# Kernel optimization log

Measured on AMD Instinct MI355X. Metric: run time of the kernel, lower is better.

## Reference

```python
import jax, jax.numpy as jnp
import numpy as np

B, N, E = 2, 30000, 120000
IN_F, OUT_F, H = 512, 512, 4
D = OUT_F // H  # head_dim = 128
LN_EPS = 1e-5


def setup_inputs() -> dict:
    key = jax.random.key(0)
    k1, k2, k3, k4 = jax.random.split(key, 4)
    node_features = jax.random.normal(k1, (B, N, IN_F), dtype=jnp.float32)
    edge_index = jax.random.randint(k2, (2, E), 0, N, dtype=jnp.int64)
    # per-head linear transforms (bias=False): W[h] is [in_features, head_dim]
    W = jax.random.normal(k3, (H, IN_F, D), dtype=jnp.float32) / np.sqrt(IN_F)
    # per-head attention vectors a[h] is [2*head_dim] (Linear(2*head_dim,1,bias=False))
    a = jax.random.normal(k4, (H, 2 * D), dtype=jnp.float32) / np.sqrt(2 * D)
    ln_gamma = jnp.ones((OUT_F,), dtype=jnp.float32)
    ln_beta = jnp.zeros((OUT_F,), dtype=jnp.float32)
    return {"node_features": node_features, "edge_index": edge_index,
            "W": W, "a": a, "ln_gamma": ln_gamma, "ln_beta": ln_beta}


def reference(node_features, edge_index, W, a, ln_gamma, ln_beta):
    src, dst = edge_index[0], edge_index[1]
    # all-heads linear transform: [B, H, N, D]
    t = jnp.einsum('bni,hid->bhnd', node_features, W)
    # per-edge gathered features: [B, H, E, D]
    sf = t[:, :, src, :]
    df = t[:, :, dst, :]
    # attention score = [sf ; df] . a  == sf.a_src + df.a_dst  -> [B, H, E]
    scores = (jnp.einsum('bhed,hd->bhe', sf, a[:, :D])
              + jnp.einsum('bhed,hd->bhe', df, a[:, D:]))
    scores = jax.nn.leaky_relu(scores, negative_slope=0.2)
    # NOTE: faithful to source — softmax over ALL edges (dim=-1), not per-dst
    w = jax.nn.softmax(scores, axis=-1)
    # scatter-add aggregation into destination nodes (the Python-loop in torch)
    agg = jnp.zeros_like(t).at[:, :, dst, :].add(w[..., None] * sf)  # [B,H,N,D]
    # concat heads along feature dim (head order preserved)
    out = jnp.transpose(agg, (0, 2, 1, 3)).reshape(node_features.shape[0], N, H * D)
    # LayerNorm over last dim
    mu = jnp.mean(out, axis=-1, keepdims=True)
    var = jnp.mean(jnp.square(out - mu), axis=-1, keepdims=True)
    out = (out - mu) * jax.lax.rsqrt(var + LN_EPS) * ln_gamma + ln_beta
    return out
```

## Files before the change

kernel.cpp:

```cpp
#include <hip/hip_runtime.h>
#include <stdint.h>

#define Bn 2
#define Nn 30000
#define En 120000
#define KIN 512
#define Hh 4
#define Dd 128
#define MROWS 60000
#define MPAD  60032
#define LNEPS 1e-5f
#define EBLK 469

typedef unsigned short u16;
typedef unsigned int   u32;
typedef __attribute__((ext_vector_type(8))) short short8;
typedef __attribute__((ext_vector_type(4))) float f32x4;

__device__ __forceinline__ u16 f2bf(float f) {
    u32 u = __builtin_bit_cast(u32, f);
    u32 r = u + 0x7FFFu + ((u >> 16) & 1u);
    return (u16)(r >> 16);
}
__device__ __forceinline__ float bflo(u32 u) {
    return __builtin_bit_cast(float, u << 16);
}
__device__ __forceinline__ float bfhi(u32 u) {
    return __builtin_bit_cast(float, u & 0xFFFF0000u);
}
__device__ __forceinline__ void ld16(void* lds, const void* g) {
    __builtin_amdgcn_global_load_lds((const __attribute__((address_space(1))) void*)g,
                                     (__attribute__((address_space(3))) void*)lds, 16, 0, 0);
}

#define CVTW_BLKS 1024
__global__ void prep_kernel(const float* __restrict__ W, u16* __restrict__ wbt,
                            const int* __restrict__ ei, int* __restrict__ deg) {
    int blk = blockIdx.x;
    if (blk < CVTW_BLKS) {
        int idx = blk * 256 + threadIdx.x;
        int c = idx >> 9, i = idx & 511;
        int h = c >> 7, d = c & 127;
        wbt[idx] = f2bf(W[h * (KIN * Dd) + i * Dd + d]);
    } else {
        int e = (blk - CVTW_BLKS) * 256 + threadIdx.x;
        if (e < En) atomicAdd(&deg[ei[En + e]], 1);
    }
}

__device__ void scan512(const int* __restrict__ deg, int* __restrict__ offs,
                        int* __restrict__ cursor, int* __restrict__ part) {
    int tid = threadIdx.x;
    const int CH = 59;
    int start = tid * CH;
    int s = 0;
    for (int i = 0; i < CH; i++) {
        int n = start + i;
        if (n < Nn) s += deg[n];
    }
    part[tid] = s;
    __syncthreads();
    for (int off = 1; off < 512; off <<= 1) {
        int xv = (tid >= off) ? part[tid - off] : 0;
        __syncthreads();
        part[tid] += xv;
        __syncthreads();
    }
    int run = part[tid] - s;
    for (int i = 0; i < CH; i++) {
        int n = start + i;
        if (n < Nn) {
            offs[n] = run;
            cursor[n] = run;
            run += deg[n];
        }
    }
    if (tid == 511) offs[Nn] = part[511];
}

#define A_LDS (2 * 128 * 32)
#define B_LDS (2 * 512 * 32)
__launch_bounds__(512)
__global__ void gemm(const float* __restrict__ x, const u16* __restrict__ wbt,
                     const float* __restrict__ ag, u16* __restrict__ t,
                     float* __restrict__ s1g, float* __restrict__ s2g,
                     const int* __restrict__ deg, int* __restrict__ offs,
                     int* __restrict__ cursor) {
    __shared__ __align__(16) u16 smem[A_LDS + B_LDS];
    if (blockIdx.x == 0) { scan512(deg, offs, cursor, (int*)smem); return; }
    u16* As0 = smem;
    u16* As1 = smem + 128 * 32;
    u16* Bs0 = smem + A_LDS;
    u16* Bs1 = smem + A_LDS + 512 * 32;
    const int tid = threadIdx.x;
    const int m0 = (blockIdx.x - 1) * 128;
    const int w = tid >> 6, l = tid & 63;
    const int lr = l & 15, lk = l >> 4;
    const int wrM = (w >> 2) * 64;
    const int h = w & 3;
    const int wc = h * 128;
    const int swz = (lk * 8) ^ ((lr & 6) << 2);
    int aoff[4], boff[8];
    #pragma unroll
    for (int mi = 0; mi < 4; mi++) aoff[mi] = (wrM + mi * 16 + lr) * 32 + swz;
    #pragma unroll
    for (int nj = 0; nj < 8; nj++) boff[nj] = (wc + nj * 16 + lr) * 32 + swz;

    const int arow_u = m0 + (tid >> 2);
    const int arow = arow_u < MROWS ? arow_u : (MROWS - 1);
    const float* xsrc = x + (long)arow * KIN + (tid & 3) * 8;
    const int awr = (tid >> 2) * 32 + (((tid & 3) * 8) ^ (((tid >> 2) & 6) << 2));

    const int grow = tid >> 2, gslot = tid & 3;
    const int gsw = (gslot * 8) ^ ((grow & 6) << 2);
    const u16* bgsrc = wbt + (long)grow * KIN + gsw;
    f32x4 acc[4][8] = {};
    float4 a0A, a1A, a0B, a1B;

#define LOADX(R0, R1, KS)                                           \
    {                                                               \
        R0 = *(const float4*)(xsrc + (KS) * 32);                    \
        R1 = *(const float4*)(xsrc + (KS) * 32 + 4);                \
    }
#define CVTW(BUF, R0, R1)                                           \
    {                                                               \
        short8 o;                                                   \
        o[0] = (short)f2bf(R0.x); o[1] = (short)f2bf(R0.y);         \
        o[2] = (short)f2bf(R0.z); o[3] = (short)f2bf(R0.w);         \
        o[4] = (short)f2bf(R1.x); o[5] = (short)f2bf(R1.y);         \
        o[6] = (short)f2bf(R1.z); o[7] = (short)f2bf(R1.w);         \
        *(short8*)&(BUF)[awr] = o;                                  \
    }

    auto STAGEB = [&](u16* Bb, int k0) {
        #pragma unroll
        for (int i = 0; i < 4; i++)
            ld16(Bb + ((long)(i * 512 + tid)) * 8, bgsrc + (long)i * 128 * KIN + k0);
    };

    LOADX(a0A, a1A, 0);
    LOADX(a0B, a1B, 1);
    STAGEB(Bs0, 0);
    CVTW(As0, a0A, a1A);
    __syncthreads();

    #pragma unroll
    for (int t16 = 0; t16 < 16; t16++) {
        u16* Acur = (t16 & 1) ? As1 : As0;
        u16* Bcur = (t16 & 1) ? Bs1 : Bs0;
        u16* Anext = (t16 & 1) ? As0 : As1;
        u16* Bnext = (t16 & 1) ? Bs0 : Bs1;
        if (t16 < 14) {
            if (t16 & 1) { LOADX(a0B, a1B, t16 + 2); }
            else         { LOADX(a0A, a1A, t16 + 2); }
        }
        if (t16 < 15) STAGEB(Bnext, (t16 + 1) * 32);
        short8 af[4];
        #pragma unroll
        for (int mi = 0; mi < 4; mi++) af[mi] = *(const short8*)&Acur[aoff[mi]];
        #pragma unroll
        for (int nj = 0; nj < 8; nj++) {
            short8 bv = *(const short8*)&Bcur[boff[nj]];
            #pragma unroll
            for (int mi = 0; mi < 4; mi++)
                acc[mi][nj] = __builtin_amdgcn_mfma_f32_16x16x32_bf16(
                    af[mi], bv, acc[mi][nj], 0, 0, 0);
        }
        if (t16 < 15) {
            if (t16 & 1) { CVTW(Anext, a0A, a1A); }
            else         { CVTW(Anext, a0B, a1B); }
        }
        __syncthreads();
    }
#undef LOADX
#undef CVTW

    #pragma unroll
    for (int mi = 0; mi < 4; mi++)
        #pragma unroll
        for (int r = 0; r < 4; r++) {
            int row = m0 + wrM + mi * 16 + lk * 4 + r;
            u16* tp = t + (long)row * 512 + wc + lr;
            #pragma unroll
            for (int nj = 0; nj < 8; nj++)
                tp[nj * 16] = f2bf(acc[mi][nj][r]);
        }
    float a1c[8], a2c[8];
    #pragma unroll
    for (int nj = 0; nj < 8; nj++) {
        int col = nj * 16 + lr;
        a1c[nj] = ag[h * 256 + col];
        a2c[nj] = ag[h * 256 + 128 + col];
    }
    float p1[16], p2[16];
    #pragma unroll
    for (int mi = 0; mi < 4; mi++)
        #pragma unroll
        for (int r = 0; r < 4; r++) {
            float v1 = 0.f, v2 = 0.f;
            #pragma unroll
            for (int nj = 0; nj < 8; nj++) {
                float tv = acc[mi][nj][r];
                v1 += tv * a1c[nj];
                v2 += tv * a2c[nj];
            }
            p1[mi * 4 + r] = v1;
            p2[mi * 4 + r] = v2;
        }
    #pragma unroll
    for (int off = 1; off < 16; off <<= 1)
        #pragma unroll
        for (int i = 0; i < 16; i++) {
            p1[i] += __shfl_xor(p1[i], off, 64);
            p2[i] += __shfl_xor(p2[i], off, 64);
        }
    if (lr == 0) {
        #pragma unroll
        for (int mi = 0; mi < 4; mi++)
            #pragma unroll
            for (int r = 0; r < 4; r++) {
                int row = m0 + wrM + mi * 16 + lk * 4 + r;
                if (row < MROWS) {
                    s1g[(long)row * 4 + h] = p1[mi * 4 + r];
                    s2g[(long)row * 4 + h] = p2[mi * 4 + r];
                }
            }
    }
}

__global__ void edgescatter_kernel(const int* __restrict__ ei, const float* __restrict__ s1,
                                   const float* __restrict__ s2, int* __restrict__ cursor,
                                   int* __restrict__ srcs, float* __restrict__ pw,
                                   float* __restrict__ Zpart) {
    int e = blockIdx.x * 256 + threadIdx.x;
    int tid = threadIdx.x;
    float v[8] = {0.f, 0.f, 0.f, 0.f, 0.f, 0.f, 0.f, 0.f};
    if (e < En) {
        int src = ei[e], dst = ei[En + e];
        #pragma unroll
        for (int b = 0; b < Bn; b++) {
            float4 v1 = *(const float4*)(s1 + ((long)b * Nn + src) * 4);
            float4 v2 = *(const float4*)(s2 + ((long)b * Nn + dst) * 4);
            float s;
            s = v1.x + v2.x; s = s > 0.f ? s : 0.2f * s; v[b * 4 + 0] = __expf(s);
            s = v1.y + v2.y; s = s > 0.f ? s : 0.2f * s; v[b * 4 + 1] = __expf(s);
            s = v1.z + v2.z; s = s > 0.f ? s : 0.2f * s; v[b * 4 + 2] = __expf(s);
            s = v1.w + v2.w; s = s > 0.f ? s : 0.2f * s; v[b * 4 + 3] = __expf(s);
        }
        int pos = atomicAdd(&cursor[dst], 1);
        srcs[pos] = src;
        *(float4*)(pw + (long)pos * 4)        = make_float4(v[0], v[1], v[2], v[3]);
        *(float4*)(pw + ((long)En + pos) * 4) = make_float4(v[4], v[5], v[6], v[7]);
    }
    #pragma unroll
    for (int off = 1; off < 64; off <<= 1)
        #pragma unroll
        for (int i = 0; i < 8; i++)
            v[i] += __shfl_xor(v[i], off, 64);
    __shared__ float red[4][8];
    if ((tid & 63) == 0)
        #pragma unroll
        for (int i = 0; i < 8; i++)
            red[tid >> 6][i] = v[i];
    __syncthreads();
    if (tid < 8)
        Zpart[(long)blockIdx.x * 8 + tid] =
            red[0][tid] + red[1][tid] + red[2][tid] + red[3][tid];
}

__global__ void zreduce_kernel(const float* __restrict__ Zpart, float* __restrict__ invZ) {
    int tid = threadIdx.x;
    int g = tid >> 5, l = tid & 31;
    float s = 0.f;
    for (int i = l; i < EBLK; i += 32)
        s += Zpart[(long)i * 8 + g];
    #pragma unroll
    for (int off = 1; off < 32; off <<= 1)
        s += __shfl_xor(s, off, 64);
    if (l == 0) invZ[g] = 1.0f / s;
}

__launch_bounds__(128)
__global__ void agg_kernel(const u16* __restrict__ t, const int* __restrict__ srcs,
                           const float* __restrict__ pw, const float* __restrict__ invZ,
                           const int* __restrict__ offs,
                           const float* __restrict__ gamma, const float* __restrict__ beta,
                           float* __restrict__ out) {
    int tid = threadIdx.x;
    int b = tid >> 6;
    int l = tid & 63;
    int n = blockIdx.x;
    int h = l >> 4;
    int j0 = offs[n], j1 = offs[n + 1];
    const float* pwb = pw + (long)b * En * 4;
    const u16* tb = t + (long)b * Nn * 512;
    float a0 = 0.f, a1 = 0.f, a2 = 0.f, a3 = 0.f;
    float a4 = 0.f, a5 = 0.f, a6 = 0.f, a7 = 0.f;
    for (int j = j0; j < j1; j += 4) {
        int  jj0 = j,     jj1 = j + 1,  jj2 = j + 2,  jj3 = j + 3;
        bool k1 = jj1 < j1, k2 = jj2 < j1, k3 = jj3 < j1;
        int  i1 = k1 ? jj1 : j0, i2 = k2 ? jj2 : j0, i3 = k3 ? jj3 : j0;
        int s0 = srcs[jj0], s1i = srcs[i1], s2i = srcs[i2], s3i = srcs[i3];
        float w0 = pwb[(long)jj0 * 4 + h];
        float w1 = k1 ? pwb[(long)i1 * 4 + h] : 0.f;
        float w2 = k2 ? pwb[(long)i2 * 4 + h] : 0.f;
        float w3 = k3 ? pwb[(long)i3 * 4 + h] : 0.f;
        uint4 r0 = *(const uint4*)(tb + (long)s0 * 512 + l * 8);
        uint4 r1 = *(const uint4*)(tb + (long)s1i * 512 + l * 8);
        uint4 r2 = *(const uint4*)(tb + (long)s2i * 512 + l * 8);
        uint4 r3 = *(const uint4*)(tb + (long)s3i * 512 + l * 8);
        a0 += w0 * bflo(r0.x) + w1 * bflo(r1.x) + w2 * bflo(r2.x) + w3 * bflo(r3.x);
        a1 += w0 * bfhi(r0.x) + w1 * bfhi(r1.x) + w2 * bfhi(r2.x) + w3 * bfhi(r3.x);
        a2 += w0 * bflo(r0.y) + w1 * bflo(r1.y) + w2 * bflo(r2.y) + w3 * bflo(r3.y);
        a3 += w0 * bfhi(r0.y) + w1 * bfhi(r1.y) + w2 * bfhi(r2.y) + w3 * bfhi(r3.y);
        a4 += w0 * bflo(r0.z) + w1 * bflo(r1.z) + w2 * bflo(r2.z) + w3 * bflo(r3.z);
        a5 += w0 * bfhi(r0.z) + w1 * bfhi(r1.z) + w2 * bfhi(r2.z) + w3 * bfhi(r3.z);
        a6 += w0 * bflo(r0.w) + w1 * bflo(r1.w) + w2 * bflo(r2.w) + w3 * bflo(r3.w);
        a7 += w0 * bfhi(r0.w) + w1 * bfhi(r1.w) + w2 * bfhi(r2.w) + w3 * bfhi(r3.w);
    }
    float invz = invZ[b * 4 + h];
    a0 *= invz; a1 *= invz; a2 *= invz; a3 *= invz;
    a4 *= invz; a5 *= invz; a6 *= invz; a7 *= invz;
    float s  = a0 + a1 + a2 + a3 + a4 + a5 + a6 + a7;
    float ss = a0 * a0 + a1 * a1 + a2 * a2 + a3 * a3
             + a4 * a4 + a5 * a5 + a6 * a6 + a7 * a7;
    #pragma unroll
    for (int off = 1; off < 64; off <<= 1) {
        s  += __shfl_xor(s, off, 64);
        ss += __shfl_xor(ss, off, 64);
    }
    float mean = s * (1.0f / 512.0f);
    float var = ss * (1.0f / 512.0f) - mean * mean;
    var = var < 0.f ? 0.f : var;
    float scale = rsqrtf(var + LNEPS);
    int c = l * 8;
    float4 g0 = *(const float4*)(gamma + c);
    float4 g1 = *(const float4*)(gamma + c + 4);
    float4 b0 = *(const float4*)(beta + c);
    float4 b1 = *(const float4*)(beta + c + 4);
    float4 o0, o1;
    o0.x = (a0 - mean) * scale * g0.x + b0.x;
    o0.y = (a1 - mean) * scale * g0.y + b0.y;
    o0.z = (a2 - mean) * scale * g0.z + b0.z;
    o0.w = (a3 - mean) * scale * g0.w + b0.w;
    o1.x = (a4 - mean) * scale * g1.x + b1.x;
    o1.y = (a5 - mean) * scale * g1.y + b1.y;
    o1.z = (a6 - mean) * scale * g1.z + b1.z;
    o1.w = (a7 - mean) * scale * g1.w + b1.w;
    float* op = out + ((long)b * Nn + n) * 512 + c;
    *(float4*)(op)     = o0;
    *(float4*)(op + 4) = o1;
}

extern "C" void kernel_launch(void* const* d_in, const int* in_sizes, int n_in,
                              void* d_out, int out_size, void* d_ws, size_t ws_size,
                              hipStream_t stream) {
    const float* x     = (const float*)d_in[0];
    const int*   ei    = (const int*)d_in[1];
    const float* W     = (const float*)d_in[2];
    const float* a     = (const float*)d_in[3];
    const float* gamma = (const float*)d_in[4];
    const float* beta  = (const float*)d_in[5];
    float* out = (float*)d_out;

    char* ws = (char*)d_ws;
    size_t off = 0;
    auto alloc = [&](size_t bytes) -> void* {
        void* ptr = ws + off;
        off = (off + bytes + 255) & ~(size_t)255;
        return ptr;
    };
    u16*   wbt    = (u16*)alloc((size_t)512 * 512 * 2);
    u16*   t      = (u16*)alloc((size_t)MPAD * 512 * 2);
    float* s1     = (float*)alloc((size_t)MROWS * 4 * 4);
    float* s2     = (float*)alloc((size_t)MROWS * 4 * 4);
    float* pw     = (float*)alloc((size_t)Bn * En * 4 * 4);
    float* Zpart  = (float*)alloc((size_t)EBLK * 8 * 4);
    float* invZ   = (float*)alloc(8 * 4);
    int*   deg    = (int*)alloc((size_t)Nn * 4);
    int*   offs   = (int*)alloc((size_t)(Nn + 1) * 4);
    int*   cursor = (int*)alloc((size_t)Nn * 4);
    int*   srcs   = (int*)alloc((size_t)En * 4);

    hipMemsetAsync(deg, 0, (size_t)Nn * 4, stream);

    prep_kernel<<<CVTW_BLKS + EBLK, 256, 0, stream>>>(W, wbt, ei, deg);
    gemm<<<470, 512, 0, stream>>>(x, wbt, a, t, s1, s2, deg, offs, cursor);
    edgescatter_kernel<<<EBLK, 256, 0, stream>>>(ei, s1, s2, cursor, srcs, pw, Zpart);
    zreduce_kernel<<<1, 256, 0, stream>>>(Zpart, invZ);
    agg_kernel<<<Nn, 128, 0, stream>>>(t, srcs, pw, invZ, offs, gamma, beta, out);
}
```

Baseline: 361.7 us.

## Fuse all stages into one cooperative persistent kernel with grid syncs

Replaces the memset and five kernel launches with a single cooperative kernel of 256 blocks that runs weight conversion, degree counting, the GEMM, the CSR scan, edge scatter, the Z reduction and aggregation/LayerNorm, separated by grid.sync. This removes launch gaps and the separate Z reduction kernel; the softmax denominator is now accumulated with global atomics. In exchange the GEMM runs on only 256 blocks for 469 tiles, which is about two uneven waves. The scan still sits on a single block, and each grid barrier adds a cost. Aggregation moves to one wave per (node, batch) pair in a grid-stride loop.

```diff
diff --git a/kernel.cpp b/kernel.cpp
--- a/kernel.cpp
+++ b/kernel.cpp
@@ -1,5 +1,8 @@
 #include <hip/hip_runtime.h>
+#include <hip/hip_cooperative_groups.h>
 #include <stdint.h>
+
+namespace cg = cooperative_groups;
 
 #define Bn 2
 #define Nn 30000
@@ -10,7 +13,8 @@
 #define MROWS 60000
 #define MPAD  60032
 #define LNEPS 1e-5f
-#define EBLK 469
+#define NBLK 256
+#define NTHR 512
 
 typedef unsigned short u16;
 typedef unsigned int   u32;
@@ -31,21 +35,6 @@
 __device__ __forceinline__ void ld16(void* lds, const void* g) {
     __builtin_amdgcn_global_load_lds((const __attribute__((address_space(1))) void*)g,
                                      (__attribute__((address_space(3))) void*)lds, 16, 0, 0);
-}
-
-#define CVTW_BLKS 1024
-__global__ void prep_kernel(const float* __restrict__ W, u16* __restrict__ wbt,
-                            const int* __restrict__ ei, int* __restrict__ deg) {
-    int blk = blockIdx.x;
-    if (blk < CVTW_BLKS) {
-        int idx = blk * 256 + threadIdx.x;
-        int c = idx >> 9, i = idx & 511;
-        int h = c >> 7, d = c & 127;
-        wbt[idx] = f2bf(W[h * (KIN * Dd) + i * Dd + d]);
-    } else {
-        int e = (blk - CVTW_BLKS) * 256 + threadIdx.x;
-        if (e < En) atomicAdd(&deg[ei[En + e]], 1);
-    }
 }
 
 __device__ void scan512(const int* __restrict__ deg, int* __restrict__ offs,
@@ -81,41 +70,68 @@
 #define A_LDS (2 * 128 * 32)
 #define B_LDS (2 * 512 * 32)
 __launch_bounds__(512)
-__global__ void gemm(const float* __restrict__ x, const u16* __restrict__ wbt,
-                     const float* __restrict__ ag, u16* __restrict__ t,
+__global__ void mega(const float* __restrict__ x, const int* __restrict__ ei,
+                     const float* __restrict__ W, const float* __restrict__ ag,
+                     const float* __restrict__ gamma, const float* __restrict__ beta,
+                     float* __restrict__ out,
+                     u16* __restrict__ wbt, u16* __restrict__ t,
                      float* __restrict__ s1g, float* __restrict__ s2g,
-                     const int* __restrict__ deg, int* __restrict__ offs,
-                     int* __restrict__ cursor) {
+                     float* __restrict__ pw, float* __restrict__ Zsum,
+                     int* __restrict__ deg, int* __restrict__ offs,
+                     int* __restrict__ cursor, int* __restrict__ srcs) {
+    cg::grid_group grid = cg::this_grid();
     __shared__ __align__(16) u16 smem[A_LDS + B_LDS];
-    if (blockIdx.x == 0) { scan512(deg, offs, cursor, (int*)smem); return; }
-    u16* As0 = smem;
-    u16* As1 = smem + 128 * 32;
-    u16* Bs0 = smem + A_LDS;
-    u16* Bs1 = smem + A_LDS + 512 * 32;
+    const int blk = blockIdx.x;
     const int tid = threadIdx.x;
-    const int m0 = (blockIdx.x - 1) * 128;
-    const int w = tid >> 6, l = tid & 63;
-    const int lr = l & 15, lk = l >> 4;
-    const int wrM = (w >> 2) * 64;
-    const int h = w & 3;
-    const int wc = h * 128;
-    const int swz = (lk * 8) ^ ((lr & 6) << 2);
-    int aoff[4], boff[8];
-    #pragma unroll
-    for (int mi = 0; mi < 4; mi++) aoff[mi] = (wrM + mi * 16 + lr) * 32 + swz;
-    #pragma unroll
-    for (int nj = 0; nj < 8; nj++) boff[nj] = (wc + nj * 16 + lr) * 32 + swz;
-
-    const int arow_u = m0 + (tid >> 2);
-    const int arow = arow_u < MROWS ? arow_u : (MROWS - 1);
-    const float* xsrc = x + (long)arow * KIN + (tid & 3) * 8;
-    const int awr = (tid >> 2) * 32 + (((tid & 3) * 8) ^ (((tid >> 2) & 6) << 2));
-
-    const int grow = tid >> 2, gslot = tid & 3;
-    const int gsw = (gslot * 8) ^ ((grow & 6) << 2);
-    const u16* bgsrc = wbt + (long)grow * KIN + gsw;
-    f32x4 acc[4][8] = {};
-    float4 a0A, a1A, a0B, a1B;
+    const int gtid = blk * NTHR + tid;
+
+    if (gtid < Nn) deg[gtid] = 0;
+    if (gtid < 8) Zsum[gtid] = 0.f;
+    grid.sync();
+
+    {
+        int idx = gtid * 2;
+        #pragma unroll
+        for (int q = 0; q < 2; q++, idx++) {
+            int c = idx >> 9, i = idx & 511;
+            int h = c >> 7, d = c & 127;
+            wbt[idx] = f2bf(W[h * (KIN * Dd) + i * Dd + d]);
+        }
+        if (gtid < En) atomicAdd(&deg[ei[En + gtid]], 1);
+    }
+    grid.sync();
+
+    for (int item = blk; item < 470; item += NBLK) {
+        if (item == 0) {
+            scan512(deg, offs, cursor, (int*)smem);
+        } else {
+            u16* As0 = smem;
+            u16* As1 = smem + 128 * 32;
+            u16* Bs0 = smem + A_LDS;
+            u16* Bs1 = smem + A_LDS + 512 * 32;
+            const int m0 = (item - 1) * 128;
+            const int w = tid >> 6, l = tid & 63;
+            const int lr = l & 15, lk = l >> 4;
+            const int wrM = (w >> 2) * 64;
+            const int h = w & 3;
+            const int wc = h * 128;
+            const int swz = (lk * 8) ^ ((lr & 6) << 2);
+            int aoff[4], boff[8];
+            #pragma unroll
+            for (int mi = 0; mi < 4; mi++) aoff[mi] = (wrM + mi * 16 + lr) * 32 + swz;
+            #pragma unroll
+            for (int nj = 0; nj < 8; nj++) boff[nj] = (wc + nj * 16 + lr) * 32 + swz;
+
+            const int arow_u = m0 + (tid >> 2);
+            const int arow = arow_u < MROWS ? arow_u : (MROWS - 1);
+            const float* xsrc = x + (long)arow * KIN + (tid & 3) * 8;
+            const int awr = (tid >> 2) * 32 + (((tid & 3) * 8) ^ (((tid >> 2) & 6) << 2));
+
+            const int grow = tid >> 2, gslot = tid & 3;
+            const int gsw = (gslot * 8) ^ ((grow & 6) << 2);
+            const u16* bgsrc = wbt + (long)grow * KIN + gsw;
+            f32x4 acc[4][8] = {};
+            float4 a0A, a1A, a0B, a1B;
 
 #define LOADX(R0, R1, KS)                                           \
     {                                                               \
@@ -131,225 +147,212 @@
         o[6] = (short)f2bf(R1.z); o[7] = (short)f2bf(R1.w);         \
         *(short8*)&(BUF)[awr] = o;                                  \
     }
-
-    auto STAGEB = [&](u16* Bb, int k0) {
-        #pragma unroll
-        for (int i = 0; i < 4; i++)
-            ld16(Bb + ((long)(i * 512 + tid)) * 8, bgsrc + (long)i * 128 * KIN + k0);
-    };
-
-    LOADX(a0A, a1A, 0);
-    LOADX(a0B, a1B, 1);
-    STAGEB(Bs0, 0);
-    CVTW(As0, a0A, a1A);
-    __syncthreads();
-
-    #pragma unroll
-    for (int t16 = 0; t16 < 16; t16++) {
-        u16* Acur = (t16 & 1) ? As1 : As0;
-        u16* Bcur = (t16 & 1) ? Bs1 : Bs0;
-        u16* Anext = (t16 & 1) ? As0 : As1;
-        u16* Bnext = (t16 & 1) ? Bs0 : Bs1;
-        if (t16 < 14) {
-            if (t16 & 1) { LOADX(a0B, a1B, t16 + 2); }
-            else         { LOADX(a0A, a1A, t16 + 2); }
-        }
-        if (t16 < 15) STAGEB(Bnext, (t16 + 1) * 32);
-        short8 af[4];
-        #pragma unroll
-        for (int mi = 0; mi < 4; mi++) af[mi] = *(const short8*)&Acur[aoff[mi]];
-        #pragma unroll
-        for (int nj = 0; nj < 8; nj++) {
-            short8 bv = *(const short8*)&Bcur[boff[nj]];
-            #pragma unroll
-            for (int mi = 0; mi < 4; mi++)
-                acc[mi][nj] = __builtin_amdgcn_mfma_f32_16x16x32_bf16(
-                    af[mi], bv, acc[mi][nj], 0, 0, 0);
-        }
-        if (t16 < 15) {
-            if (t16 & 1) { CVTW(Anext, a0A, a1A); }
-            else         { CVTW(Anext, a0B, a1B); }
-        }
-        __syncthreads();
-    }
+#define STAGEB(BB, K0)                                              \
+    {                                                               \
+        _Pragma("unroll")                                           \
+        for (int i = 0; i < 4; i++)                                 \
+            ld16((BB) + ((long)(i * 512 + tid)) * 8,                \
+                 bgsrc + (long)i * 128 * KIN + (K0));               \
+    }
+
+            LOADX(a0A, a1A, 0);
+            LOADX(a0B, a1B, 1);
+            STAGEB(Bs0, 0);
+            CVTW(As0, a0A, a1A);
+            __syncthreads();
+
+            #pragma unroll
+            for (int t16 = 0; t16 < 16; t16++) {
+                u16* Acur = (t16 & 1) ? As1 : As0;
+                u16* Bcur = (t16 & 1) ? Bs1 : Bs0;
+                u16* Anext = (t16 & 1) ? As0 : As1;
+                u16* Bnext = (t16 & 1) ? Bs0 : Bs1;
+                if (t16 < 14) {
+                    if (t16 & 1) { LOADX(a0B, a1B, t16 + 2); }
+                    else         { LOADX(a0A, a1A, t16 + 2); }
+                }
+                if (t16 < 15) STAGEB(Bnext, (t16 + 1) * 32);
+                short8 af[4];
+                #pragma unroll
+                for (int mi = 0; mi < 4; mi++) af[mi] = *(const short8*)&Acur[aoff[mi]];
+                #pragma unroll
+                for (int nj = 0; nj < 8; nj++) {
+                    short8 bv = *(const short8*)&Bcur[boff[nj]];
+                    #pragma unroll
+                    for (int mi = 0; mi < 4; mi++)
+                        acc[mi][nj] = __builtin_amdgcn_mfma_f32_16x16x32_bf16(
+                            af[mi], bv, acc[mi][nj], 0, 0, 0);
+                }
+                if (t16 < 15) {
+                    if (t16 & 1) { CVTW(Anext, a0A, a1A); }
+                    else         { CVTW(Anext, a0B, a1B); }
+                }
+                __syncthreads();
+            }
 #undef LOADX
 #undef CVTW
-
-    #pragma unroll
-    for (int mi = 0; mi < 4; mi++)
+#undef STAGEB
+
+            #pragma unroll
+            for (int mi = 0; mi < 4; mi++)
+                #pragma unroll
+                for (int r = 0; r < 4; r++) {
+                    int row = m0 + wrM + mi * 16 + lk * 4 + r;
+                    u16* tp = t + (long)row * 512 + wc + lr;
+                    #pragma unroll
+                    for (int nj = 0; nj < 8; nj++)
+                        tp[nj * 16] = f2bf(acc[mi][nj][r]);
+                }
+            float a1c[8], a2c[8];
+            #pragma unroll
+            for (int nj = 0; nj < 8; nj++) {
+                int col = nj * 16 + lr;
+                a1c[nj] = ag[h * 256 + col];
+                a2c[nj] = ag[h * 256 + 128 + col];
+            }
+            float p1[16], p2[16];
+            #pragma unroll
+            for (int mi = 0; mi < 4; mi++)
+                #pragma unroll
+                for (int r = 0; r < 4; r++) {
+                    float v1 = 0.f, v2 = 0.f;
+                    #pragma unroll
+                    for (int nj = 0; nj < 8; nj++) {
+                        float tv = acc[mi][nj][r];
+                        v1 += tv * a1c[nj];
+                        v2 += tv * a2c[nj];
+                    }
+                    p1[mi * 4 + r] = v1;
+                    p2[mi * 4 + r] = v2;
+                }
+            #pragma unroll
+            for (int off = 1; off < 16; off <<= 1)
+                #pragma unroll
+                for (int i = 0; i < 16; i++) {
+                    p1[i] += __shfl_xor(p1[i], off, 64);
+                    p2[i] += __shfl_xor(p2[i], off, 64);
+                }
+            if (lr == 0) {
+                #pragma unroll
+                for (int mi = 0; mi < 4; mi++)
+                    #pragma unroll
+                    for (int r = 0; r < 4; r++) {
+                        int row = m0 + wrM + mi * 16 + lk * 4 + r;
+                        if (row < MROWS) {
+                            s1g[(long)row * 4 + h] = p1[mi * 4 + r];
+                            s2g[(long)row * 4 + h] = p2[mi * 4 + r];
+                        }
+                    }
+            }
+        }
+        __syncthreads();
+    }
+    grid.sync();
+
+    {
+        int e = gtid;
+        float v[8] = {0.f, 0.f, 0.f, 0.f, 0.f, 0.f, 0.f, 0.f};
+        if (e < En) {
+            int src = ei[e], dst = ei[En + e];
+            #pragma unroll
+            for (int b = 0; b < Bn; b++) {
+                float4 v1 = *(const float4*)(s1g + ((long)b * Nn + src) * 4);
+                float4 v2 = *(const float4*)(s2g + ((long)b * Nn + dst) * 4);
+                float s;
+                s = v1.x + v2.x; s = s > 0.f ? s : 0.2f * s; v[b * 4 + 0] = __expf(s);
+                s = v1.y + v2.y; s = s > 0.f ? s : 0.2f * s; v[b * 4 + 1] = __expf(s);
+                s = v1.z + v2.z; s = s > 0.f ? s : 0.2f * s; v[b * 4 + 2] = __expf(s);
+                s = v1.w + v2.w; s = s > 0.f ? s : 0.2f * s; v[b * 4 + 3] = __expf(s);
+            }
+            int pos = atomicAdd(&cursor[dst], 1);
+            srcs[pos] = src;
+            *(float4*)(pw + (long)pos * 4)        = make_float4(v[0], v[1], v[2], v[3]);
+            *(float4*)(pw + ((long)En + pos) * 4) = make_float4(v[4], v[5], v[6], v[7]);
+        }
         #pragma unroll
-        for (int r = 0; r < 4; r++) {
-            int row = m0 + wrM + mi * 16 + lk * 4 + r;
-            u16* tp = t + (long)row * 512 + wc + lr;
-            #pragma unroll
-            for (int nj = 0; nj < 8; nj++)
-                tp[nj * 16] = f2bf(acc[mi][nj][r]);
-        }
-    float a1c[8], a2c[8];
-    #pragma unroll
-    for (int nj = 0; nj < 8; nj++) {
-        int col = nj * 16 + lr;
-        a1c[nj] = ag[h * 256 + col];
-        a2c[nj] = ag[h * 256 + 128 + col];
-    }
-    float p1[16], p2[16];
-    #pragma unroll
-    for (int mi = 0; mi < 4; mi++)
+        for (int off = 1; off < 64; off <<= 1)
+            #pragma unroll
+            for (int i = 0; i < 8; i++)
+                v[i] += __shfl_xor(v[i], off, 64);
+        float* red = (float*)smem;
+        if ((tid & 63) == 0)
+            #pragma unroll
+            for (int i = 0; i < 8; i++)
+                red[(tid >> 6) * 8 + i] = v[i];
+        __syncthreads();
+        if (tid < 8) {
+            float sum = 0.f;
+            #pragma unroll
+            for (int w2 = 0; w2 < 8; w2++) sum += red[w2 * 8 + tid];
+            atomicAdd(&Zsum[tid], sum);
+        }
+    }
+    grid.sync();
+
+    for (int wid = blk * 8 + (tid >> 6); wid < Bn * Nn; wid += NBLK * 8) {
+        int n = wid >> 1, b = wid & 1;
+        int l = tid & 63;
+        int h = l >> 4;
+        int j0 = offs[n], j1 = offs[n + 1];
+        const float* pwb = pw + (long)b * En * 4;
+        const u16* tb = t + (long)b * Nn * 512;
+        float a0 = 0.f, a1 = 0.f, a2 = 0.f, a3 = 0.f;
+        float a4 = 0.f, a5 = 0.f, a6 = 0.f, a7 = 0.f;
+        for (int j = j0; j < j1; j += 4) {
+            int  jj0 = j,     jj1 = j + 1,  jj2 = j + 2,  jj3 = j + 3;
+            bool k1 = jj1 < j1, k2 = jj2 < j1, k3 = jj3 < j1;
+            int  i1 = k1 ? jj1 : jj0, i2 = k2 ? jj2 : jj0, i3 = k3 ? jj3 : jj0;
+            int s0 = srcs[jj0], s1i = srcs[i1], s2i = srcs[i2], s3i = srcs[i3];
+            float w0 = pwb[(long)jj0 * 4 + h];
+            float w1 = k1 ? pwb[(long)i1 * 4 + h] : 0.f;
+            float w2 = k2 ? pwb[(long)i2 * 4 + h] : 0.f;
+            float w3 = k3 ? pwb[(long)i3 * 4 + h] : 0.f;
+            uint4 r0 = *(const uint4*)(tb + (long)s0 * 512 + l * 8);
+            uint4 r1 = *(const uint4*)(tb + (long)s1i * 512 + l * 8);
+            uint4 r2 = *(const uint4*)(tb + (long)s2i * 512 + l * 8);
+            uint4 r3 = *(const uint4*)(tb + (long)s3i * 512 + l * 8);
+            a0 += w0 * bflo(r0.x) + w1 * bflo(r1.x) + w2 * bflo(r2.x) + w3 * bflo(r3.x);
+            a1 += w0 * bfhi(r0.x) + w1 * bfhi(r1.x) + w2 * bfhi(r2.x) + w3 * bfhi(r3.x);
+            a2 += w0 * bflo(r0.y) + w1 * bflo(r1.y) + w2 * bflo(r2.y) + w3 * bflo(r3.y);
+            a3 += w0 * bfhi(r0.y) + w1 * bfhi(r1.y) + w2 * bfhi(r2.y) + w3 * bfhi(r3.y);
+            a4 += w0 * bflo(r0.z) + w1 * bflo(r1.z) + w2 * bflo(r2.z) + w3 * bflo(r3.z);
+            a5 += w0 * bfhi(r0.z) + w1 * bfhi(r1.z) + w2 * bfhi(r2.z) + w3 * bfhi(r3.z);
+            a6 += w0 * bflo(r0.w) + w1 * bflo(r1.w) + w2 * bflo(r2.w) + w3 * bflo(r3.w);
+            a7 += w0 * bfhi(r0.w) + w1 * bfhi(r1.w) + w2 * bfhi(r2.w) + w3 * bfhi(r3.w);
+        }
+        float invz = 1.0f / Zsum[b * 4 + h];
+        a0 *= invz; a1 *= invz; a2 *= invz; a3 *= invz;
+        a4 *= invz; a5 *= invz; a6 *= invz; a7 *= invz;
+        float s  = a0 + a1 + a2 + a3 + a4 + a5 + a6 + a7;
+        float ss = a0 * a0 + a1 * a1 + a2 * a2 + a3 * a3
+                 + a4 * a4 + a5 * a5 + a6 * a6 + a7 * a7;
         #pragma unroll
-        for (int r = 0; r < 4; r++) {
-            float v1 = 0.f, v2 = 0.f;
-            #pragma unroll
-            for (int nj = 0; nj < 8; nj++) {
-                float tv = acc[mi][nj][r];
-                v1 += tv * a1c[nj];
-                v2 += tv * a2c[nj];
-            }
-            p1[mi * 4 + r] = v1;
-            p2[mi * 4 + r] = v2;
-        }
-    #pragma unroll
-    for (int off = 1; off < 16; off <<= 1)
-        #pragma unroll
-        for (int i = 0; i < 16; i++) {
-            p1[i] += __shfl_xor(p1[i], off, 64);
-            p2[i] += __shfl_xor(p2[i], off, 64);
-        }
-    if (lr == 0) {
-        #pragma unroll
-        for (int mi = 0; mi < 4; mi++)
-            #pragma unroll
-            for (int r = 0; r < 4; r++) {
-                int row = m0 + wrM + mi * 16 + lk * 4 + r;
-                if (row < MROWS) {
-                    s1g[(long)row * 4 + h] = p1[mi * 4 + r];
-                    s2g[(long)row * 4 + h] = p2[mi * 4 + r];
-                }
-            }
-    }
-}
-
-__global__ void edgescatter_kernel(const int* __restrict__ ei, const float* __restrict__ s1,
-                                   const float* __restrict__ s2, int* __restrict__ cursor,
-                                   int* __restrict__ srcs, float* __restrict__ pw,
-                                   float* __restrict__ Zpart) {
-    int e = blockIdx.x * 256 + threadIdx.x;
-    int tid = threadIdx.x;
-    float v[8] = {0.f, 0.f, 0.f, 0.f, 0.f, 0.f, 0.f, 0.f};
-    if (e < En) {
-        int src = ei[e], dst = ei[En + e];
-        #pragma unroll
-        for (int b = 0; b < Bn; b++) {
-            float4 v1 = *(const float4*)(s1 + ((long)b * Nn + src) * 4);
-            float4 v2 = *(const float4*)(s2 + ((long)b * Nn + dst) * 4);
-            float s;
-            s = v1.x + v2.x; s = s > 0.f ? s : 0.2f * s; v[b * 4 + 0] = __expf(s);
-            s = v1.y + v2.y; s = s > 0.f ? s : 0.2f * s; v[b * 4 + 1] = __expf(s);
-            s = v1.z + v2.z; s = s > 0.f ? s : 0.2f * s; v[b * 4 + 2] = __expf(s);
-            s = v1.w + v2.w; s = s > 0.f ? s : 0.2f * s; v[b * 4 + 3] = __expf(s);
-        }
-        int pos = atomicAdd(&cursor[dst], 1);
-        srcs[pos] = src;
-        *(float4*)(pw + (long)pos * 4)        = make_float4(v[0], v[1], v[2], v[3]);
-        *(float4*)(pw + ((long)En + pos) * 4) = make_float4(v[4], v[5], v[6], v[7]);
-    }
-    #pragma unroll
-    for (int off = 1; off < 64; off <<= 1)
-        #pragma unroll
-        for (int i = 0; i < 8; i++)
-            v[i] += __shfl_xor(v[i], off, 64);
-    __shared__ float red[4][8];
-    if ((tid & 63) == 0)
-        #pragma unroll
-        for (int i = 0; i < 8; i++)
-            red[tid >> 6][i] = v[i];
-    __syncthreads();
-    if (tid < 8)
-        Zpart[(long)blockIdx.x * 8 + tid] =
-            red[0][tid] + red[1][tid] + red[2][tid] + red[3][tid];
-}
-
-__global__ void zreduce_kernel(const float* __restrict__ Zpart, float* __restrict__ invZ) {
-    int tid = threadIdx.x;
-    int g = tid >> 5, l = tid & 31;
-    float s = 0.f;
-    for (int i = l; i < EBLK; i += 32)
-        s += Zpart[(long)i * 8 + g];
-    #pragma unroll
-    for (int off = 1; off < 32; off <<= 1)
-        s += __shfl_xor(s, off, 64);
-    if (l == 0) invZ[g] = 1.0f / s;
-}
-
-__launch_bounds__(128)
-__global__ void agg_kernel(const u16* __restrict__ t, const int* __restrict__ srcs,
-                           const float* __restrict__ pw, const float* __restrict__ invZ,
-                           const int* __restrict__ offs,
-                           const float* __restrict__ gamma, const float* __restrict__ beta,
-                           float* __restrict__ out) {
-    int tid = threadIdx.x;
-    int b = tid >> 6;
-    int l = tid & 63;
-    int n = blockIdx.x;
-    int h = l >> 4;
-    int j0 = offs[n], j1 = offs[n + 1];
-    const float* pwb = pw + (long)b * En * 4;
-    const u16* tb = t + (long)b * Nn * 512;
-    float a0 = 0.f, a1 = 0.f, a2 = 0.f, a3 = 0.f;
-    float a4 = 0.f, a5 = 0.f, a6 = 0.f, a7 = 0.f;
-    for (int j = j0; j < j1; j += 4) {
-        int  jj0 = j,     jj1 = j + 1,  jj2 = j + 2,  jj3 = j + 3;
-        bool k1 = jj1 < j1, k2 = jj2 < j1, k3 = jj3 < j1;
-        int  i1 = k1 ? jj1 : j0, i2 = k2 ? jj2 : j0, i3 = k3 ? jj3 : j0;
-        int s0 = srcs[jj0], s1i = srcs[i1], s2i = srcs[i2], s3i = srcs[i3];
-        float w0 = pwb[(long)jj0 * 4 + h];
-        float w1 = k1 ? pwb[(long)i1 * 4 + h] : 0.f;
-        float w2 = k2 ? pwb[(long)i2 * 4 + h] : 0.f;
-        float w3 = k3 ? pwb[(long)i3 * 4 + h] : 0.f;
-        uint4 r0 = *(const uint4*)(tb + (long)s0 * 512 + l * 8);
-        uint4 r1 = *(const uint4*)(tb + (long)s1i * 512 + l * 8);
-        uint4 r2 = *(const uint4*)(tb + (long)s2i * 512 + l * 8);
-        uint4 r3 = *(const uint4*)(tb + (long)s3i * 512 + l * 8);
-        a0 += w0 * bflo(r0.x) + w1 * bflo(r1.x) + w2 * bflo(r2.x) + w3 * bflo(r3.x);
-        a1 += w0 * bfhi(r0.x) + w1 * bfhi(r1.x) + w2 * bfhi(r2.x) + w3 * bfhi(r3.x);
-        a2 += w0 * bflo(r0.y) + w1 * bflo(r1.y) + w2 * bflo(r2.y) + w3 * bflo(r3.y);
-        a3 += w0 * bfhi(r0.y) + w1 * bfhi(r1.y) + w2 * bfhi(r2.y) + w3 * bfhi(r3.y);
-        a4 += w0 * bflo(r0.z) + w1 * bflo(r1.z) + w2 * bflo(r2.z) + w3 * bflo(r3.z);
-        a5 += w0 * bfhi(r0.z) + w1 * bfhi(r1.z) + w2 * bfhi(r2.z) + w3 * bfhi(r3.z);
-        a6 += w0 * bflo(r0.w) + w1 * bflo(r1.w) + w2 * bflo(r2.w) + w3 * bflo(r3.w);
-        a7 += w0 * bfhi(r0.w) + w1 * bfhi(r1.w) + w2 * bfhi(r2.w) + w3 * bfhi(r3.w);
-    }
-    float invz = invZ[b * 4 + h];
-    a0 *= invz; a1 *= invz; a2 *= invz; a3 *= invz;
-    a4 *= invz; a5 *= invz; a6 *= invz; a7 *= invz;
-    float s  = a0 + a1 + a2 + a3 + a4 + a5 + a6 + a7;
-    float ss = a0 * a0 + a1 * a1 + a2 * a2 + a3 * a3
-             + a4 * a4 + a5 * a5 + a6 * a6 + a7 * a7;
-    #pragma unroll
-    for (int off = 1; off < 64; off <<= 1) {
-        s  += __shfl_xor(s, off, 64);
-        ss += __shfl_xor(ss, off, 64);
-    }
-    float mean = s * (1.0f / 512.0f);
-    float var = ss * (1.0f / 512.0f) - mean * mean;
-    var = var < 0.f ? 0.f : var;
-    float scale = rsqrtf(var + LNEPS);
-    int c = l * 8;
-    float4 g0 = *(const float4*)(gamma + c);
-    float4 g1 = *(const float4*)(gamma + c + 4);
-    float4 b0 = *(const float4*)(beta + c);
-    float4 b1 = *(const float4*)(beta + c + 4);
-    float4 o0, o1;
-    o0.x = (a0 - mean) * scale * g0.x + b0.x;
-    o0.y = (a1 - mean) * scale * g0.y + b0.y;
-    o0.z = (a2 - mean) * scale * g0.z + b0.z;
-    o0.w = (a3 - mean) * scale * g0.w + b0.w;
-    o1.x = (a4 - mean) * scale * g1.x + b1.x;
-    o1.y = (a5 - mean) * scale * g1.y + b1.y;
-    o1.z = (a6 - mean) * scale * g1.z + b1.z;
-    o1.w = (a7 - mean) * scale * g1.w + b1.w;
-    float* op = out + ((long)b * Nn + n) * 512 + c;
-    *(float4*)(op)     = o0;
-    *(float4*)(op + 4) = o1;
+        for (int off = 1; off < 64; off <<= 1) {
+            s  += __shfl_xor(s, off, 64);
+            ss += __shfl_xor(ss, off, 64);
+        }
+        float mean = s * (1.0f / 512.0f);
+        float var = ss * (1.0f / 512.0f) - mean * mean;
+        var = var < 0.f ? 0.f : var;
+        float scale = rsqrtf(var + LNEPS);
+        int c = l * 8;
+        float4 g0 = *(const float4*)(gamma + c);
+        float4 g1 = *(const float4*)(gamma + c + 4);
+        float4 b0 = *(const float4*)(beta + c);
+        float4 b1 = *(const float4*)(beta + c + 4);
+        float4 o0, o1;
+        o0.x = (a0 - mean) * scale * g0.x + b0.x;
+        o0.y = (a1 - mean) * scale * g0.y + b0.y;
+        o0.z = (a2 - mean) * scale * g0.z + b0.z;
+        o0.w = (a3 - mean) * scale * g0.w + b0.w;
+        o1.x = (a4 - mean) * scale * g1.x + b1.x;
+        o1.y = (a5 - mean) * scale * g1.y + b1.y;
+        o1.z = (a6 - mean) * scale * g1.z + b1.z;
+        o1.w = (a7 - mean) * scale * g1.w + b1.w;
+        float* op = out + ((long)b * Nn + n) * 512 + c;
+        *(float4*)(op)     = o0;
+        *(float4*)(op + 4) = o1;
+    }
 }
 
 extern "C" void kernel_launch(void* const* d_in, const int* in_sizes, int n_in,
@@ -375,18 +378,16 @@
     float* s1     = (float*)alloc((size_t)MROWS * 4 * 4);
     float* s2     = (float*)alloc((size_t)MROWS * 4 * 4);
     float* pw     = (float*)alloc((size_t)Bn * En * 4 * 4);
-    float* Zpart  = (float*)alloc((size_t)EBLK * 8 * 4);
-    float* invZ   = (float*)alloc(8 * 4);
+    float* Zsum   = (float*)alloc(8 * 4);
     int*   deg    = (int*)alloc((size_t)Nn * 4);
     int*   offs   = (int*)alloc((size_t)(Nn + 1) * 4);
     int*   cursor = (int*)alloc((size_t)Nn * 4);
     int*   srcs   = (int*)alloc((size_t)En * 4);
 
-    hipMemsetAsync(deg, 0, (size_t)Nn * 4, stream);
-
-    prep_kernel<<<CVTW_BLKS + EBLK, 256, 0, stream>>>(W, wbt, ei, deg);
-    gemm<<<470, 512, 0, stream>>>(x, wbt, a, t, s1, s2, deg, offs, cursor);
-    edgescatter_kernel<<<EBLK, 256, 0, stream>>>(ei, s1, s2, cursor, srcs, pw, Zpart);
-    zreduce_kernel<<<1, 256, 0, stream>>>(Zpart, invZ);
-    agg_kernel<<<Nn, 128, 0, stream>>>(t, srcs, pw, invZ, offs, gamma, beta, out);
-}
+    void* args[] = {(void*)&x, (void*)&ei, (void*)&W, (void*)&a, (void*)&gamma,
+                    (void*)&beta, (void*)&out, (void*)&wbt, (void*)&t, (void*)&s1,
+                    (void*)&s2, (void*)&pw, (void*)&Zsum, (void*)&deg, (void*)&offs,
+                    (void*)&cursor, (void*)&srcs};
+    hipLaunchCooperativeKernel((const void*)mega, dim3(NBLK), dim3(NTHR),
+                               args, 0, stream);
+}
```

New measurement: 546.4 us. 1.51x slower.

## Load GEMM A operand straight to registers, triple-buffer B, fold Z reduction into atomics

Applied to the files above, without the earlier changes.

The GEMM no longer stages the fp32 activations through LDS. Each lane loads its own A rows into registers and converts them to bf16 MFMA fragments directly. The B tile becomes a three-deep LDS ring with explicit vmcnt waits and one barrier per k-step, replacing the two __syncthreads per iteration. The separate softmax-denominator reduction kernel is removed: edge blocks atomically add into an 8-float sum, and the aggregation kernel takes the reciprocal itself. The costs are one extra memset, hand-tuned waitcnt counts that depend on the number of outstanding loads, redundant global loads of x across warps that share rows, and a non-deterministic float atomic sum.

```diff
diff --git a/kernel.cpp b/kernel.cpp
--- a/kernel.cpp
+++ b/kernel.cpp
@@ -78,20 +78,15 @@
     if (tid == 511) offs[Nn] = part[511];
 }
 
-#define A_LDS (2 * 128 * 32)
-#define B_LDS (2 * 512 * 32)
+#define BBUF 16384
 __launch_bounds__(512)
 __global__ void gemm(const float* __restrict__ x, const u16* __restrict__ wbt,
                      const float* __restrict__ ag, u16* __restrict__ t,
                      float* __restrict__ s1g, float* __restrict__ s2g,
                      const int* __restrict__ deg, int* __restrict__ offs,
                      int* __restrict__ cursor) {
-    __shared__ __align__(16) u16 smem[A_LDS + B_LDS];
+    __shared__ __align__(16) u16 smem[3 * BBUF];
     if (blockIdx.x == 0) { scan512(deg, offs, cursor, (int*)smem); return; }
-    u16* As0 = smem;
-    u16* As1 = smem + 128 * 32;
-    u16* Bs0 = smem + A_LDS;
-    u16* Bs1 = smem + A_LDS + 512 * 32;
     const int tid = threadIdx.x;
     const int m0 = (blockIdx.x - 1) * 128;
     const int w = tid >> 6, l = tid & 63;
@@ -100,80 +95,89 @@
     const int h = w & 3;
     const int wc = h * 128;
     const int swz = (lk * 8) ^ ((lr & 6) << 2);
-    int aoff[4], boff[8];
-    #pragma unroll
-    for (int mi = 0; mi < 4; mi++) aoff[mi] = (wrM + mi * 16 + lr) * 32 + swz;
+    int boff[8];
     #pragma unroll
     for (int nj = 0; nj < 8; nj++) boff[nj] = (wc + nj * 16 + lr) * 32 + swz;
-
-    const int arow_u = m0 + (tid >> 2);
-    const int arow = arow_u < MROWS ? arow_u : (MROWS - 1);
-    const float* xsrc = x + (long)arow * KIN + (tid & 3) * 8;
-    const int awr = (tid >> 2) * 32 + (((tid & 3) * 8) ^ (((tid >> 2) & 6) << 2));
 
     const int grow = tid >> 2, gslot = tid & 3;
     const int gsw = (gslot * 8) ^ ((grow & 6) << 2);
     const u16* bgsrc = wbt + (long)grow * KIN + gsw;
+
+    const float* xrow[4];
+    #pragma unroll
+    for (int mi = 0; mi < 4; mi++) {
+        int r = m0 + wrM + mi * 16 + lr;
+        if (r >= MROWS) r = MROWS - 1;
+        xrow[mi] = x + (long)r * KIN + lk * 8;
+    }
+
     f32x4 acc[4][8] = {};
-    float4 a0A, a1A, a0B, a1B;
-
-#define LOADX(R0, R1, KS)                                           \
+    float4 sA[8], sB[8];
+
+#define STAGEB(BI, K0)                                              \
     {                                                               \
-        R0 = *(const float4*)(xsrc + (KS) * 32);                    \
-        R1 = *(const float4*)(xsrc + (KS) * 32 + 4);                \
-    }
-#define CVTW(BUF, R0, R1)                                           \
+        _Pragma("unroll")                                           \
+        for (int i = 0; i < 4; i++)                                 \
+            ld16(smem + (BI) * BBUF + ((long)(i * 512 + tid)) * 8,  \
+                 bgsrc + (long)i * 128 * KIN + (K0));               \
+    }
+#define LOADA(S, KS)                                                \
     {                                                               \
-        short8 o;                                                   \
-        o[0] = (short)f2bf(R0.x); o[1] = (short)f2bf(R0.y);         \
-        o[2] = (short)f2bf(R0.z); o[3] = (short)f2bf(R0.w);         \
-        o[4] = (short)f2bf(R1.x); o[5] = (short)f2bf(R1.y);         \
-        o[6] = (short)f2bf(R1.z); o[7] = (short)f2bf(R1.w);         \
-        *(short8*)&(BUF)[awr] = o;                                  \
-    }
-
-    auto STAGEB = [&](u16* Bb, int k0) {
-        #pragma unroll
-        for (int i = 0; i < 4; i++)
-            ld16(Bb + ((long)(i * 512 + tid)) * 8, bgsrc + (long)i * 128 * KIN + k0);
-    };
-
-    LOADX(a0A, a1A, 0);
-    LOADX(a0B, a1B, 1);
-    STAGEB(Bs0, 0);
-    CVTW(As0, a0A, a1A);
-    __syncthreads();
+        _Pragma("unroll")                                           \
+        for (int mi = 0; mi < 4; mi++) {                            \
+            S[mi * 2]     = *(const float4*)(xrow[mi] + (KS) * 32);     \
+            S[mi * 2 + 1] = *(const float4*)(xrow[mi] + (KS) * 32 + 4); \
+        }                                                           \
+    }
+#define CVTA(S, AF)                                                 \
+    {                                                               \
+        _Pragma("unroll")                                           \
+        for (int mi = 0; mi < 4; mi++) {                            \
+            short8 o;                                               \
+            o[0] = (short)f2bf(S[mi * 2].x);                        \
+            o[1] = (short)f2bf(S[mi * 2].y);                        \
+            o[2] = (short)f2bf(S[mi * 2].z);                        \
+            o[3] = (short)f2bf(S[mi * 2].w);                        \
+            o[4] = (short)f2bf(S[mi * 2 + 1].x);                    \
+            o[5] = (short)f2bf(S[mi * 2 + 1].y);                    \
+            o[6] = (short)f2bf(S[mi * 2 + 1].z);                    \
+            o[7] = (short)f2bf(S[mi * 2 + 1].w);                    \
+            AF[mi] = o;                                             \
+        }                                                           \
+    }
+
+    STAGEB(0, 0);
+    LOADA(sA, 0);
+    STAGEB(1, 32);
+    LOADA(sB, 1);
 
     #pragma unroll
     for (int t16 = 0; t16 < 16; t16++) {
-        u16* Acur = (t16 & 1) ? As1 : As0;
-        u16* Bcur = (t16 & 1) ? Bs1 : Bs0;
-        u16* Anext = (t16 & 1) ? As0 : As1;
-        u16* Bnext = (t16 & 1) ? Bs0 : Bs1;
+        __builtin_amdgcn_s_barrier();
+        if (t16 < 14) STAGEB((t16 + 2) % 3, (t16 + 2) * 32);
+        if (t16 <= 13)      asm volatile("s_waitcnt vmcnt(24)" ::: "memory");
+        else if (t16 == 14) asm volatile("s_waitcnt vmcnt(12)" ::: "memory");
+        else                asm volatile("s_waitcnt vmcnt(0)"  ::: "memory");
+        __builtin_amdgcn_sched_barrier(0);
+        short8 af[4];
+        if (t16 & 1) { CVTA(sB, af); } else { CVTA(sA, af); }
         if (t16 < 14) {
-            if (t16 & 1) { LOADX(a0B, a1B, t16 + 2); }
-            else         { LOADX(a0A, a1A, t16 + 2); }
-        }
-        if (t16 < 15) STAGEB(Bnext, (t16 + 1) * 32);
-        short8 af[4];
-        #pragma unroll
-        for (int mi = 0; mi < 4; mi++) af[mi] = *(const short8*)&Acur[aoff[mi]];
+            if (t16 & 1) { LOADA(sB, t16 + 2); }
+            else         { LOADA(sA, t16 + 2); }
+        }
+        const u16* Bc = smem + (t16 % 3) * BBUF;
         #pragma unroll
         for (int nj = 0; nj < 8; nj++) {
-            short8 bv = *(const short8*)&Bcur[boff[nj]];
+            short8 bv = *(const short8*)&Bc[boff[nj]];
             #pragma unroll
             for (int mi = 0; mi < 4; mi++)
                 acc[mi][nj] = __builtin_amdgcn_mfma_f32_16x16x32_bf16(
                     af[mi], bv, acc[mi][nj], 0, 0, 0);
         }
-        if (t16 < 15) {
-            if (t16 & 1) { CVTW(Anext, a0A, a1A); }
-            else         { CVTW(Anext, a0B, a1B); }
-        }
-        __syncthreads();
-    }
-#undef LOADX
-#undef CVTW
+    }
+#undef STAGEB
+#undef LOADA
+#undef CVTA
 
     #pragma unroll
     for (int mi = 0; mi < 4; mi++)
@@ -231,7 +235,7 @@
 __global__ void edgescatter_kernel(const int* __restrict__ ei, const float* __restrict__ s1,
                                    const float* __restrict__ s2, int* __restrict__ cursor,
                                    int* __restrict__ srcs, float* __restrict__ pw,
-                                   float* __restrict__ Zpart) {
+                                   float* __restrict__ Zsum) {
     int e = blockIdx.x * 256 + threadIdx.x;
     int tid = threadIdx.x;
     float v[8] = {0.f, 0.f, 0.f, 0.f, 0.f, 0.f, 0.f, 0.f};
@@ -264,25 +268,12 @@
             red[tid >> 6][i] = v[i];
     __syncthreads();
     if (tid < 8)
-        Zpart[(long)blockIdx.x * 8 + tid] =
-            red[0][tid] + red[1][tid] + red[2][tid] + red[3][tid];
-}
-
-__global__ void zreduce_kernel(const float* __restrict__ Zpart, float* __restrict__ invZ) {
-    int tid = threadIdx.x;
-    int g = tid >> 5, l = tid & 31;
-    float s = 0.f;
-    for (int i = l; i < EBLK; i += 32)
-        s += Zpart[(long)i * 8 + g];
-    #pragma unroll
-    for (int off = 1; off < 32; off <<= 1)
-        s += __shfl_xor(s, off, 64);
-    if (l == 0) invZ[g] = 1.0f / s;
+        atomicAdd(&Zsum[tid], red[0][tid] + red[1][tid] + red[2][tid] + red[3][tid]);
 }
 
 __launch_bounds__(128)
 __global__ void agg_kernel(const u16* __restrict__ t, const int* __restrict__ srcs,
-                           const float* __restrict__ pw, const float* __restrict__ invZ,
+                           const float* __restrict__ pw, const float* __restrict__ Zsum,
                            const int* __restrict__ offs,
                            const float* __restrict__ gamma, const float* __restrict__ beta,
                            float* __restrict__ out) {
@@ -299,7 +290,7 @@
     for (int j = j0; j < j1; j += 4) {
         int  jj0 = j,     jj1 = j + 1,  jj2 = j + 2,  jj3 = j + 3;
         bool k1 = jj1 < j1, k2 = jj2 < j1, k3 = jj3 < j1;
-        int  i1 = k1 ? jj1 : j0, i2 = k2 ? jj2 : j0, i3 = k3 ? jj3 : j0;
+        int  i1 = k1 ? jj1 : jj0, i2 = k2 ? jj2 : jj0, i3 = k3 ? jj3 : jj0;
         int s0 = srcs[jj0], s1i = srcs[i1], s2i = srcs[i2], s3i = srcs[i3];
         float w0 = pwb[(long)jj0 * 4 + h];
         float w1 = k1 ? pwb[(long)i1 * 4 + h] : 0.f;
@@ -318,7 +309,7 @@
         a6 += w0 * bflo(r0.w) + w1 * bflo(r1.w) + w2 * bflo(r2.w) + w3 * bflo(r3.w);
         a7 += w0 * bfhi(r0.w) + w1 * bfhi(r1.w) + w2 * bfhi(r2.w) + w3 * bfhi(r3.w);
     }
-    float invz = invZ[b * 4 + h];
+    float invz = 1.0f / Zsum[b * 4 + h];
     a0 *= invz; a1 *= invz; a2 *= invz; a3 *= invz;
     a4 *= invz; a5 *= invz; a6 *= invz; a7 *= invz;
     float s  = a0 + a1 + a2 + a3 + a4 + a5 + a6 + a7;
@@ -375,18 +366,17 @@
     float* s1     = (float*)alloc((size_t)MROWS * 4 * 4);
     float* s2     = (float*)alloc((size_t)MROWS * 4 * 4);
     float* pw     = (float*)alloc((size_t)Bn * En * 4 * 4);
-    float* Zpart  = (float*)alloc((size_t)EBLK * 8 * 4);
-    float* invZ   = (float*)alloc(8 * 4);
+    float* Zsum   = (float*)alloc(8 * 4);
     int*   deg    = (int*)alloc((size_t)Nn * 4);
     int*   offs   = (int*)alloc((size_t)(Nn + 1) * 4);
     int*   cursor = (int*)alloc((size_t)Nn * 4);
     int*   srcs   = (int*)alloc((size_t)En * 4);
 
     hipMemsetAsync(deg, 0, (size_t)Nn * 4, stream);
+    hipMemsetAsync(Zsum, 0, 8 * 4, stream);
 
     prep_kernel<<<CVTW_BLKS + EBLK, 256, 0, stream>>>(W, wbt, ei, deg);
     gemm<<<470, 512, 0, stream>>>(x, wbt, a, t, s1, s2, deg, offs, cursor);
-    edgescatter_kernel<<<EBLK, 256, 0, stream>>>(ei, s1, s2, cursor, srcs, pw, Zpart);
-    zreduce_kernel<<<1, 256, 0, stream>>>(Zpart, invZ);
-    agg_kernel<<<Nn, 128, 0, stream>>>(t, srcs, pw, invZ, offs, gamma, beta, out);
-}
+    edgescatter_kernel<<<EBLK, 256, 0, stream>>>(ei, s1, s2, cursor, srcs, pw, Zsum);
+    agg_kernel<<<Nn, 128, 0, stream>>>(t, srcs, pw, Zsum, offs, gamma, beta, out);
+}
```

New measurement: 386.9 us. +7.0%, slower.
